# Optimization experiments

Hardware: AMD Instinct MI355X
Metric: run time of the kernel (lower is better)

The kernel has to match this reference:

```python
import jax, jax.numpy as jnp
import numpy as np

N = 50000      # nodes
E = 800000     # edges
IN_DIM = 16
D = 128        # latent_dim == d_model == num_heads*d_head
H = 8
DH = 16
DFF = 512
L = 3          # n_layers
CLAMP = 5.0
EPS = 1e-5


def _layer_norm(x, g, b):
    mu = jnp.mean(x, axis=-1, keepdims=True)
    var = jnp.mean((x - mu) ** 2, axis=-1, keepdims=True)
    return (x - mu) * jax.lax.rsqrt(var + EPS) * g + b


def setup_inputs() -> dict:
    key = jax.random.key(0)
    ks = jax.random.split(key, 16)
    def w(k, shape, fan_in):
        return jax.random.normal(k, shape, dtype=jnp.float32) * (1.0 / np.sqrt(fan_in))
    inp = {
        "nf": jax.random.normal(ks[0], (N, IN_DIM), dtype=jnp.float32),
        "src": jax.random.randint(ks[1], (E,), 0, N, dtype=jnp.int32),
        "dst": jax.random.randint(ks[2], (E,), 0, N, dtype=jnp.int32),
        "enc_W": w(ks[3], (D, IN_DIM), IN_DIM),
        "enc_b": jnp.zeros((D,), jnp.float32),
        "Wq": w(ks[4], (L, H * DH, D), D),
        "Wk": w(ks[5], (L, H * DH, D), D),
        "Wv": w(ks[6], (L, H * DH, D), D),
        "Wo": w(ks[7], (L, D, H * DH), H * DH),
        "ln1_g": jnp.ones((L, D), jnp.float32),
        "ln1_b": jnp.zeros((L, D), jnp.float32),
        "ffn_W1": w(ks[8], (L, DFF, D), D),
        "ffn_b1": jnp.zeros((L, DFF), jnp.float32),
        "ffn_W2": w(ks[9], (L, D, DFF), DFF),
        "ffn_b2": jnp.zeros((L, D), jnp.float32),
        "ln2_g": jnp.ones((L, D), jnp.float32),
        "ln2_b": jnp.zeros((L, D), jnp.float32),
        "dec_W": w(ks[10], (1, D), D),
        "dec_b": jnp.zeros((1,), jnp.float32),
    }
    return inp


def reference(nf, src, dst, enc_W, enc_b, Wq, Wk, Wv, Wo, ln1_g, ln1_b,
              ffn_W1, ffn_b1, ffn_W2, ffn_b2, ln2_g, ln2_b, dec_W, dec_b):
    h = nf @ enc_W.T + enc_b                       # [N, D]
    scale = 1.0 / np.sqrt(DH)
    for l in range(L):
        q = h @ Wq[l].T                            # [N, H*DH]
        k = h @ Wk[l].T
        v = h @ Wv[l].T
        qe = q[dst].reshape(E, H, DH)              # per-edge gather (dst query)
        ke = k[src].reshape(E, H, DH)
        u = jnp.sum(qe * ke, axis=-1) * scale      # [E, H]
        u = jnp.clip(u, -CLAMP, CLAMP)
        # edge_softmax: normalize over edges sharing the same dst node
        m = jax.ops.segment_max(u, dst, num_segments=N)   # [N, H]
        e = jnp.exp(u - m[dst])
        s = jax.ops.segment_sum(e, dst, num_segments=N)   # [N, H]
        a = e / s[dst]                             # [E, H]
        av = a[..., None] * v[src].reshape(E, H, DH)      # [E, H, DH]
        sum_av = jax.ops.segment_sum(av.reshape(E, H * DH), dst, num_segments=N)
        uh = sum_av @ Wo[l].T                      # [N, D]
        h1 = _layer_norm(h + uh, ln1_g[l], ln1_b[l])
        f = jax.nn.relu(h1 @ ffn_W1[l].T + ffn_b1[l]) @ ffn_W2[l].T + ffn_b2[l]
        h = _layer_norm(h1 + f, ln2_g[l], ln2_b[l])
    pred = h @ dec_W.T + dec_b                     # [N, 1]
    # BasicReadout('mean') over the single batched graph -> [1, 1]
    return jnp.mean(pred, axis=0, keepdims=True)
```

## Files before the change

### kernel.cpp

```cpp
#include <hip/hip_runtime.h>
#include <math.h>

static constexpr int D   = 128;
static constexpr int DFF = 512;
static constexpr int LAYERS = 3;
static constexpr float CLAMP_V = 5.0f;
static constexpr float LN_EPS = 1e-5f;

typedef unsigned short u16;
typedef unsigned int   u32;
typedef short bf16x8 __attribute__((ext_vector_type(8)));
typedef float f32x4  __attribute__((ext_vector_type(4)));

__device__ inline float4 ld4(const float* p){ return *reinterpret_cast<const float4*>(p); }
__device__ inline u16 f2bf(float f){ u32 u = __float_as_uint(f); return (u16)((u + 0x7fff + ((u>>16)&1)) >> 16); }
__device__ inline float bl(u32 u){ return __uint_as_float(u << 16); }
__device__ inline float bh(u32 u){ return __uint_as_float(u & 0xffff0000u); }

__device__ inline void gload_lds16(const void* g, void* l) {
  __builtin_amdgcn_global_load_lds(
      (const __attribute__((address_space(1))) void*)g,
      (__attribute__((address_space(3))) void*)l, 16, 0, 0);
}

__global__ __launch_bounds__(256) void count_kernel(const int* __restrict__ dst,
                                                    int* __restrict__ deg, int E)
{
  int e = blockIdx.x*256 + threadIdx.x;
  if (e < E) atomicAdd(&deg[dst[e]], 1);
}

__global__ __launch_bounds__(256) void scan_bsum(const int* __restrict__ deg,
                                                 int* __restrict__ bsum, int N)
{
  const int i0 = blockIdx.x*1024 + threadIdx.x*4;
  int s = 0;
  if (i0 + 3 < N) { int4 v = *(const int4*)&deg[i0]; s = v.x+v.y+v.z+v.w; }
  else { for (int t = 0; t < 4; t++) if (i0+t < N) s += deg[i0+t]; }
  #pragma unroll
  for (int off = 1; off < 64; off <<= 1) s += __shfl_xor(s, off);
  __shared__ int ws_[4];
  if ((threadIdx.x & 63) == 0) ws_[threadIdx.x >> 6] = s;
  __syncthreads();
  if (threadIdx.x == 0) bsum[blockIdx.x] = ws_[0]+ws_[1]+ws_[2]+ws_[3];
}

__global__ __launch_bounds__(64) void scan_bbase(int* __restrict__ bsum, int NB)
{
  const int tid = threadIdx.x;
  int base = 0;
  for (int c = 0; c < NB; c += 64) {
    const int idx = c + tid;
    int v = (idx < NB) ? bsum[idx] : 0;
    const int orig = v;
    #pragma unroll
    for (int off = 1; off < 64; off <<= 1) {
      int t = __shfl_up(v, off);
      if (tid >= off) v += t;
    }
    if (idx < NB) bsum[idx] = base + v - orig;
    base += __shfl(v, 63);
  }
}

__global__ __launch_bounds__(256) void scan_write(const int* __restrict__ deg,
    const int* __restrict__ bbase, int* __restrict__ offs, int* __restrict__ cursor, int N)
{
  const int i0 = blockIdx.x*1024 + threadIdx.x*4;
  int v[4] = {0,0,0,0};
  if (i0 + 3 < N) { int4 t = *(const int4*)&deg[i0]; v[0]=t.x; v[1]=t.y; v[2]=t.z; v[3]=t.w; }
  else { for (int t = 0; t < 4; t++) if (i0+t < N) v[t] = deg[i0+t]; }
  const int s = v[0]+v[1]+v[2]+v[3];
  const int lane = threadIdx.x & 63, w = threadIdx.x >> 6;
  int inc = s;
  #pragma unroll
  for (int off = 1; off < 64; off <<= 1) {
    int t = __shfl_up(inc, off);
    if (lane >= off) inc += t;
  }
  __shared__ int wsum[4];
  if (lane == 63) wsum[w] = inc;
  __syncthreads();
  int wb = 0;
  for (int t = 0; t < 4; t++) if (t < w) wb += wsum[t];
  int run = bbase[blockIdx.x] + wb + inc - s;
  #pragma unroll
  for (int t = 0; t < 4; t++) {
    if (i0 + t < N) { offs[i0+t] = run; cursor[i0+t] = run; run += v[t]; }
  }
  if (i0 <= N-1 && N-1 < i0+4) offs[N] = run;
}

__global__ __launch_bounds__(256) void fill_kernel(const int* __restrict__ dst,
    const int* __restrict__ src, int* __restrict__ cursor, int* __restrict__ csr_src, int E)
{
  int e = blockIdx.x*256 + threadIdx.x;
  if (e < E) {
    int p = atomicAdd(&cursor[dst[e]], 1);
    csr_src[p] = src[e];
  }
}

__global__ __launch_bounds__(256) void convert_weights(
    const float* __restrict__ Wq, const float* __restrict__ Wk, const float* __restrict__ Wv,
    const float* __restrict__ Wo, const float* __restrict__ W1, const float* __restrict__ W2,
    u16* __restrict__ out)
{
  const int SQKV = 3*384*128;
  const int SWO  = 3*128*128;
  const int SW1  = 3*512*128;
  const int SW2  = 3*128*512;
  int i = blockIdx.x*256 + threadIdx.x;
  if (i >= SQKV+SWO+SW1+SW2) return;
  float v;
  if (i < SQKV) {
    int l = i / (384*128), rem = i % (384*128);
    int row = rem / 128, col = rem % 128;
    const float* W = (row < 128) ? Wq : ((row < 256) ? Wk : Wv);
    v = W[(size_t)l*128*128 + (size_t)(row & 127)*128 + col];
  } else if (i < SQKV+SWO) {
    v = Wo[i - SQKV];
  } else if (i < SQKV+SWO+SW1) {
    v = W1[i - SQKV - SWO];
  } else {
    v = W2[i - SQKV - SWO - SW1];
  }
  out[i] = f2bf(v);
}

__global__ __launch_bounds__(256) void encoder_kernel(
    const float* __restrict__ nf, const float* __restrict__ W,
    const float* __restrict__ b, float* __restrict__ h, u16* __restrict__ hb, int N)
{
  int n = blockIdx.x*2 + (threadIdx.x >> 7);
  int d = threadIdx.x & 127;
  if (n >= N) return;
  const float* nr = nf + (size_t)n*16;
  const float* wr = W  + (size_t)d*16;
  float s = b[d];
  #pragma unroll
  for (int kk = 0; kk < 16; kk++) s = fmaf(nr[kk], wr[kk], s);
  h[(size_t)n*D + d]  = s;
  hb[(size_t)n*D + d] = f2bf(s);
}

__device__ inline void mfma_step128(const u16* __restrict__ la, const u16* __restrict__ lb,
                                    int lane, int wr, int wc, f32x4 (&acc)[4][4])
{
  #pragma unroll
  for (int k2 = 0; k2 < 2; k2++) {
    bf16x8 af[4], bfr[4];
    const int kq = k2*4 + (lane >> 4);
    #pragma unroll
    for (int mi = 0; mi < 4; mi++) {
      const int r = wr*64 + mi*16 + (lane & 15);
      af[mi] = *(const bf16x8*)&la[r*64 + ((kq ^ (r & 7)) << 3)];
    }
    #pragma unroll
    for (int ni = 0; ni < 4; ni++) {
      const int r = wc*64 + ni*16 + (lane & 15);
      bfr[ni] = *(const bf16x8*)&lb[r*64 + ((kq ^ (r & 7)) << 3)];
    }
    #pragma unroll
    for (int mi = 0; mi < 4; mi++)
      #pragma unroll
      for (int ni = 0; ni < 4; ni++)
        acc[mi][ni] = __builtin_amdgcn_mfma_f32_16x16x32_bf16(af[mi], bfr[ni], acc[mi][ni], 0, 0, 0);
  }
}

__device__ inline void mfma_stage64(const u16* __restrict__ Atile, const u16* __restrict__ Btile,
                                    int lane, int wr, int wc, int kabase, f32x4 (&acc)[2][4])
{
  #pragma unroll
  for (int k2 = 0; k2 < 2; k2++) {
    const int kql = k2*4 + (lane >> 4);
    const int kqa = kabase + kql;
    bf16x8 af[2], bfr[4];
    #pragma unroll
    for (int mi = 0; mi < 2; mi++) {
      const int r = wr*32 + mi*16 + (lane & 15);
      const int slot = ((kqa & 7) ^ (r & 7)) | (kqa & 8);
      af[mi] = *(const bf16x8*)&Atile[r*128 + slot*8];
    }
    #pragma unroll
    for (int ni = 0; ni < 4; ni++) {
      const int r = wc*64 + ni*16 + (lane & 15);
      bfr[ni] = *(const bf16x8*)&Btile[r*64 + ((kql ^ (r & 7)) << 3)];
    }
    #pragma unroll
    for (int mi = 0; mi < 2; mi++)
      #pragma unroll
      for (int ni = 0; ni < 4; ni++)
        acc[mi][ni] = __builtin_amdgcn_mfma_f32_16x16x32_bf16(af[mi], bfr[ni], acc[mi][ni], 0, 0, 0);
  }
}

__global__ __launch_bounds__(256) void gemm_qkv(
    const u16* __restrict__ A, const u16* __restrict__ B,
    float* __restrict__ qf, u16* __restrict__ kvb, int M)
{
  __shared__ u16 lA[2][128*64];
  __shared__ u16 lW[128*64];
  const int m0 = blockIdx.x * 128;
  const int tid = threadIdx.x, lane = tid & 63, wid = tid >> 6;
  const int wr = wid >> 1, wc = wid & 1;
  const int ldrow = lane >> 3;
  const int gran  = (lane & 7) ^ ldrow;

  auto issueA = [&](int ks) {
    const int k0 = ks*64 + gran*8;
    #pragma unroll
    for (int is = 0; is < 4; is++) {
      const int r = wid*32 + is*8;
      int gm = m0 + r + ldrow; if (gm >= M) gm = M - 1;
      gload_lds16(A + (size_t)gm*128 + k0, &lA[ks][r*64]);
    }
  };
  auto issueW = [&](int s) {
    const u16* Bm = B + (size_t)(s >> 1)*128*128;
    const int k0 = (s & 1)*64 + gran*8;
    #pragma unroll
    for (int is = 0; is < 4; is++) {
      const int r = wid*32 + is*8;
      gload_lds16(Bm + (size_t)(r + ldrow)*128 + k0, &lW[r*64]);
    }
  };

  issueA(0); issueA(1);

  f32x4 acc[4][4];
  const int rbase = m0 + wr*64 + ((lane >> 4) << 2);
  const int cbase = wc*64 + (lane & 15);

  #pragma unroll
  for (int s = 0; s < 6; s++) {
    issueW(s);
    asm volatile("s_waitcnt vmcnt(0)" ::: "memory");
    __syncthreads();
    if ((s & 1) == 0) {
      #pragma unroll
      for (int i = 0; i < 4; i++)
        #pragma unroll
        for (int j = 0; j < 4; j++) { acc[i][j][0]=0.f; acc[i][j][1]=0.f; acc[i][j][2]=0.f; acc[i][j][3]=0.f; }
    }
    mfma_step128(lA[s & 1], lW, lane, wr, wc, acc);
    if (s & 1) {
      const int mat = s >> 1;
      #pragma unroll
      for (int ni = 0; ni < 4; ni++) {
        const int col = cbase + ni*16;
        #pragma unroll
        for (int mi = 0; mi < 4; mi++) {
          #pragma unroll
          for (int r = 0; r < 4; r++) {
            const int gm = rbase + mi*16 + r;
            if (gm < M) {
              if (mat == 0) qf[(size_t)gm*128 + col] = acc[mi][ni][r];
              else          kvb[(size_t)gm*256 + (mat-1)*128 + col] = f2bf(acc[mi][ni][r]);
            }
          }
        }
      }
    }
    if (s < 5) __syncthreads();
  }
}

__global__ __launch_bounds__(256) void ffn_fused(
    const u16* __restrict__ savb, const u16* __restrict__ Wo,
    const u16* __restrict__ W1,   const u16* __restrict__ W2,
    const float* __restrict__ ln1g, const float* __restrict__ ln1b,
    const float* __restrict__ b1,   const float* __restrict__ b2,
    const float* __restrict__ ln2g, const float* __restrict__ ln2b,
    float* __restrict__ hf, u16* __restrict__ hb, int M)
{
  __shared__ u16 lB[128*64];
  __shared__ u16 h1s[64*128];
  __shared__ u16 fs[64*128];
  __shared__ float lsum[64][2];
  __shared__ float lsq[64][2];

  const int tid  = threadIdx.x;
  const int lane = tid & 63;
  const int wid  = tid >> 6;
  const int wr   = wid >> 1, wc = wid & 1;
  const int m0   = blockIdx.x * 64;

  const int ldrow = lane >> 3;
  const int gran  = (lane & 7) ^ ldrow;

  const int rbase_l = wr*32 + ((lane >> 4) << 2);
  const int cbase   = wc*64 + (lane & 15);

  auto stage_issue = [&](int s) {
    #pragma unroll
    for (int is = 0; is < 4; is++) {
      const int r = wid*32 + is*8;
      const u16* gp;
      if (s < 2) gp = Wo + (size_t)(r + ldrow)*128 + s*64;
      else {
        const int t = s - 2, c = t >> 2, k = t & 3;
        gp = (k < 2) ? (W1 + (size_t)(c*128 + r + ldrow)*128 + k*64)
                     : (W2 + (size_t)(r + ldrow)*512 + c*128 + (k-2)*64);
      }
      gload_lds16(gp + gran*8, &lB[r*64]);
    }
  };

  #pragma unroll
  for (int is = 0; is < 4; is++) {
    const int r0 = wid*16 + is*4;
    const int rr = r0 + (lane >> 4);
    int gm = m0 + rr; if (gm >= M) gm = M - 1;
    const int gsrc = ((lane & 7) ^ (rr & 7)) | (lane & 8);
    gload_lds16(savb + (size_t)gm*128 + gsrc*8, &fs[r0*128]);
  }

  f32x4 acc1[2][4], acc2[2][4], acc3[2][4];
  #pragma unroll
  for (int i = 0; i < 2; i++)
    #pragma unroll
    for (int j = 0; j < 4; j++) {
      acc1[i][j][0]=0.f; acc1[i][j][1]=0.f; acc1[i][j][2]=0.f; acc1[i][j][3]=0.f;
      acc3[i][j][0]=0.f; acc3[i][j][1]=0.f; acc3[i][j][2]=0.f; acc3[i][j][3]=0.f;
    }

  #pragma unroll
  for (int s = 0; s < 18; s++) {
    stage_issue(s);
    asm volatile("s_waitcnt vmcnt(0)" ::: "memory");
    __syncthreads();

    if (s >= 2 && ((s - 2) & 3) == 0) {
      #pragma unroll
      for (int i = 0; i < 2; i++)
        #pragma unroll
        for (int j = 0; j < 4; j++) { acc2[i][j][0]=0.f; acc2[i][j][1]=0.f; acc2[i][j][2]=0.f; acc2[i][j][3]=0.f; }
    }

    if (s < 2)
      mfma_stage64(fs,  lB, lane, wr, wc, (s & 1)*8, acc1);
    else if (((s - 2) & 3) < 2)
      mfma_stage64(h1s, lB, lane, wr, wc, (s & 1)*8, acc2);
    else
      mfma_stage64(fs,  lB, lane, wr, wc, (s & 1)*8, acc3);

    if (s == 1) {
      #pragma unroll
      for (int mi = 0; mi < 2; mi++) {
        #pragma unroll
        for (int r = 0; r < 4; r++) {
          const int lrow = rbase_l + mi*16 + r;
          int gr = m0 + lrow; if (gr >= M) gr = M - 1;
          float ps = 0.f, pq = 0.f;
          #pragma unroll
          for (int ni = 0; ni < 4; ni++) {
            const int col = cbase + ni*16;
            float x = acc1[mi][ni][r] + hf[(size_t)gr*128 + col];
            acc1[mi][ni][r] = x;
            ps += x; pq += x*x;
          }
          #pragma unroll
          for (int off = 1; off < 16; off <<= 1) { ps += __shfl_xor(ps, off); pq += __shfl_xor(pq, off); }
          if ((lane & 15) == 0) { lsum[lrow][wc] = ps; lsq[lrow][wc] = pq; }
        }
      }
      __syncthreads();
      #pragma unroll
      for (int mi = 0; mi < 2; mi++) {
        #pragma unroll
        for (int r = 0; r < 4; r++) {
          const int lrow = rbase_l + mi*16 + r;
          const float mean = (lsum[lrow][0] + lsum[lrow][1]) * (1.0f/128.0f);
          float var = (lsq[lrow][0] + lsq[lrow][1]) * (1.0f/128.0f) - mean*mean;
          const float rstd = rsqrtf(fmaxf(var, 0.f) + LN_EPS);
          #pragma unroll
          for (int ni = 0; ni < 4; ni++) {
            const int col = cbase + ni*16;
            float o = (acc1[mi][ni][r] - mean) * rstd * ln1g[col] + ln1b[col];
            acc1[mi][ni][r] = o;
            const int g16 = col >> 3;
            const int slot = ((g16 & 7) ^ (lrow & 7)) | (g16 & 8);
            h1s[lrow*128 + slot*8 + (col & 7)] = f2bf(o);
          }
        }
      }
    } else if (s >= 2 && ((s - 2) & 3) == 1) {
      const int c = (s - 2) >> 2;
      #pragma unroll
      for (int mi = 0; mi < 2; mi++) {
        #pragma unroll
        for (int r = 0; r < 4; r++) {
          const int lrow = rbase_l + mi*16 + r;
          #pragma unroll
          for (int ni = 0; ni < 4; ni++) {
            const int col = cbase + ni*16;
            float v = fmaxf(acc2[mi][ni][r] + b1[c*128 + col], 0.f);
            const int g16 = col >> 3;
            const int slot = ((g16 & 7) ^ (lrow & 7)) | (g16 & 8);
            fs[lrow*128 + slot*8 + (col & 7)] = f2bf(v);
          }
        }
      }
    }

    if (s < 17) __syncthreads();
  }

  #pragma unroll
  for (int mi = 0; mi < 2; mi++) {
    #pragma unroll
    for (int r = 0; r < 4; r++) {
      const int lrow = rbase_l + mi*16 + r;
      float ps = 0.f, pq = 0.f;
      #pragma unroll
      for (int ni = 0; ni < 4; ni++) {
        const int col = cbase + ni*16;
        float x = acc3[mi][ni][r] + b2[col] + acc1[mi][ni][r];
        acc3[mi][ni][r] = x;
        ps += x; pq += x*x;
      }
      #pragma unroll
      for (int off = 1; off < 16; off <<= 1) { ps += __shfl_xor(ps, off); pq += __shfl_xor(pq, off); }
      if ((lane & 15) == 0) { lsum[lrow][wc] = ps; lsq[lrow][wc] = pq; }
    }
  }
  __syncthreads();
  #pragma unroll
  for (int mi = 0; mi < 2; mi++) {
    #pragma unroll
    for (int r = 0; r < 4; r++) {
      const int lrow = rbase_l + mi*16 + r;
      const int grow = m0 + lrow;
      if (grow >= M) continue;
      const float mean = (lsum[lrow][0] + lsum[lrow][1]) * (1.0f/128.0f);
      float var = (lsq[lrow][0] + lsq[lrow][1]) * (1.0f/128.0f) - mean*mean;
      const float rstd = rsqrtf(fmaxf(var, 0.f) + LN_EPS);
      #pragma unroll
      for (int ni = 0; ni < 4; ni++) {
        const int col = cbase + ni*16;
        float o = (acc3[mi][ni][r] - mean) * rstd * ln2g[col] + ln2b[col];
        hf[(size_t)grow*128 + col] = o;
        hb[(size_t)grow*128 + col] = f2bf(o);
      }
    }
  }
}

__global__ __launch_bounds__(256) void attn_kernel(
    const float* __restrict__ q, const u16* __restrict__ kv,
    const int* __restrict__ offs, const int* __restrict__ csr_src,
    u16* __restrict__ outb, int N)
{
  const int tid = threadIdx.x;
  const int j   = tid & 15;
  const int n   = blockIdx.x*16 + (tid >> 4);
  if (n >= N) return;

  float qreg[8];
  *(float4*)&qreg[0] = ld4(&q[(size_t)n*128 + j*8]);
  *(float4*)&qreg[4] = ld4(&q[(size_t)n*128 + j*8 + 4]);

  const int start = offs[n];
  const int deg   = offs[n+1] - start;

  float s = 0.f;
  float acc[8] = {0,0,0,0,0,0,0,0};
  const int gb = tid & 48;

  for (int base = 0; base < deg; base += 16) {
    const int myidx = base + j;
    const int sn_mine = (myidx < deg) ? csr_src[start + myidx] : 0;
    const int cnt = (deg - base < 16) ? (deg - base) : 16;

    for (int b2 = 0; b2 < cnt; b2 += 8) {
      const int m8 = cnt - b2;
      uint4 K4[8], V4[8];
      #pragma unroll
      for (int u = 0; u < 8; u++) {
        const int sel = b2 + ((u < m8) ? u : 0);
        const int sn = __shfl(sn_mine, gb + sel);
        const u16* row = kv + (size_t)sn*256 + j*8;
        K4[u] = *(const uint4*)row;
        V4[u] = *(const uint4*)(row + 128);
      }
      #pragma unroll
      for (int u = 0; u < 8; u++) {
        if (u < m8) {
          float d = bl(K4[u].x)*qreg[0] + bh(K4[u].x)*qreg[1]
                  + bl(K4[u].y)*qreg[2] + bh(K4[u].y)*qreg[3]
                  + bl(K4[u].z)*qreg[4] + bh(K4[u].z)*qreg[5]
                  + bl(K4[u].w)*qreg[6] + bh(K4[u].w)*qreg[7];
          d += __shfl_xor(d, 1);
          float uu = fminf(fmaxf(d * 0.25f, -CLAMP_V), CLAMP_V);
          float e = __expf(uu - CLAMP_V);
          s += e;
          acc[0] = fmaf(e, bl(V4[u].x), acc[0]);
          acc[1] = fmaf(e, bh(V4[u].x), acc[1]);
          acc[2] = fmaf(e, bl(V4[u].y), acc[2]);
          acc[3] = fmaf(e, bh(V4[u].y), acc[3]);
          acc[4] = fmaf(e, bl(V4[u].z), acc[4]);
          acc[5] = fmaf(e, bh(V4[u].z), acc[5]);
          acc[6] = fmaf(e, bl(V4[u].w), acc[6]);
          acc[7] = fmaf(e, bh(V4[u].w), acc[7]);
        }
      }
    }
  }

  const float rs = (deg > 0) ? (1.0f / s) : 0.f;
  u16 o[8];
  #pragma unroll
  for (int t = 0; t < 8; t++) o[t] = f2bf(acc[t] * rs);
  *(uint4*)&outb[(size_t)n*128 + j*8] = *(const uint4*)o;
}

__global__ __launch_bounds__(256) void dec_partial(const float* __restrict__ h,
    const float* __restrict__ W, float* __restrict__ partials, int N)
{
  float acc = 0.f;
  for (int n = blockIdx.x*256 + threadIdx.x; n < N; n += 256*256) {
    const float* hr = h + (size_t)n*D;
    float s = 0.f;
    #pragma unroll
    for (int t = 0; t < 32; t++) {
      float4 hv = ld4(&hr[t*4]); float4 wv = ld4(&W[t*4]);
      s += hv.x*wv.x + hv.y*wv.y + hv.z*wv.z + hv.w*wv.w;
    }
    acc += s;
  }
  #pragma unroll
  for (int off = 1; off < 64; off <<= 1) acc += __shfl_xor(acc, off);
  __shared__ float red[4];
  int lane = threadIdx.x & 63, w = threadIdx.x >> 6;
  if (lane == 0) red[w] = acc;
  __syncthreads();
  if (threadIdx.x == 0) partials[blockIdx.x] = red[0]+red[1]+red[2]+red[3];
}

__global__ __launch_bounds__(256) void dec_final(const float* __restrict__ partials,
    const float* __restrict__ decb, float* __restrict__ out, int N)
{
  float a = partials[threadIdx.x];
  #pragma unroll
  for (int off = 1; off < 64; off <<= 1) a += __shfl_xor(a, off);
  __shared__ float red[4];
  int lane = threadIdx.x & 63, w = threadIdx.x >> 6;
  if (lane == 0) red[w] = a;
  __syncthreads();
  if (threadIdx.x == 0) out[0] = (red[0]+red[1]+red[2]+red[3]) / (float)N + decb[0];
}

extern "C" void kernel_launch(void* const* d_in, const int* in_sizes, int n_in,
                              void* d_out, int out_size, void* d_ws, size_t ws_size,
                              hipStream_t stream)
{
  const float* nf   = (const float*)d_in[0];
  const int*   src  = (const int*)  d_in[1];
  const int*   dst  = (const int*)  d_in[2];
  const float* encW = (const float*)d_in[3];
  const float* encb = (const float*)d_in[4];
  const float* Wq   = (const float*)d_in[5];
  const float* Wk   = (const float*)d_in[6];
  const float* Wv   = (const float*)d_in[7];
  const float* Wo   = (const float*)d_in[8];
  const float* ln1g = (const float*)d_in[9];
  const float* ln1b = (const float*)d_in[10];
  const float* W1   = (const float*)d_in[11];
  const float* b1   = (const float*)d_in[12];
  const float* W2   = (const float*)d_in[13];
  const float* b2   = (const float*)d_in[14];
  const float* ln2g = (const float*)d_in[15];
  const float* ln2b = (const float*)d_in[16];
  const float* decW = (const float*)d_in[17];
  const float* decb = (const float*)d_in[18];
  float* out = (float*)d_out;

  const int N = in_sizes[0] / 16;
  const int E = in_sizes[1];
  const int NB = (N + 1023) / 1024;

  float* ws   = (float*)d_ws;
  float* h    = ws;
  float* q    = h  + (size_t)N*128;
  u16*  hb    = (u16*)(q + (size_t)N*128);
  u16*  kvb   = hb  + (size_t)N*128;
  u16*  savb  = kvb + (size_t)N*256;
  int* deg    = (int*)(savb + (size_t)N*128);
  int* offs   = deg + N;
  int* cursor = offs + N + 1;
  int* csr    = cursor + N;
  int* bsum   = csr + E;
  float* partials = (float*)(bsum + ((NB + 255) & ~255));
  u16* wbuf   = (u16*)(partials + 512);
  u16* wqkv   = wbuf;
  u16* wo_b   = wbuf + 147456;
  u16* w1_b   = wbuf + 196608;
  u16* w2_b   = wbuf + 393216;

  hipMemsetAsync(deg, 0, sizeof(int)*N, stream);
  count_kernel<<<(E+255)/256, 256, 0, stream>>>(dst, deg, E);
  scan_bsum<<<NB, 256, 0, stream>>>(deg, bsum, N);
  scan_bbase<<<1, 64, 0, stream>>>(bsum, NB);
  scan_write<<<NB, 256, 0, stream>>>(deg, bsum, offs, cursor, N);
  fill_kernel<<<(E+255)/256, 256, 0, stream>>>(dst, src, cursor, csr, E);

  convert_weights<<<(589824+255)/256, 256, 0, stream>>>(Wq, Wk, Wv, Wo, W1, W2, wbuf);

  encoder_kernel<<<(N+1)/2, 256, 0, stream>>>(nf, encW, encb, h, hb, N);

  const int gmx = (N + 127)/128;
  for (int l = 0; l < LAYERS; l++) {
    const u16* wqkv_l = wqkv + (size_t)l*384*128;
    const u16* wo_l   = wo_b + (size_t)l*128*128;
    const u16* w1_l   = w1_b + (size_t)l*512*128;
    const u16* w2_l   = w2_b + (size_t)l*128*512;

    gemm_qkv<<<gmx, 256, 0, stream>>>(hb, wqkv_l, q, kvb, N);

    attn_kernel<<<(N+15)/16, 256, 0, stream>>>(q, kvb, offs, csr, savb, N);

    ffn_fused<<<(N+63)/64, 256, 0, stream>>>(
        savb, wo_l, w1_l, w2_l,
        ln1g + l*D, ln1b + l*D, b1 + l*DFF, b2 + l*D, ln2g + l*D, ln2b + l*D,
        h, hb, N);
  }

  dec_partial<<<256, 256, 0, stream>>>(h, decW, partials, N);
  dec_final<<<1, 256, 0, stream>>>(partials, decb, out, N);
}
```

Baseline: 545.4 us.

## Fuse next layer's QKV projection into FFN kernel epilogue

The FFN kernel now keeps the layer-norm output as bf16 in shared memory and immediately multiplies it by the next layer's Q/K/V weights, writing q and kv directly. The standalone QKV GEMM is launched only once, for the first layer. This removes two kernel launches and the write and re-read of the bf16 hidden state between kernels. In exchange the FFN kernel gets longer and uses more registers, and it no longer writes hb. The QKV stage uses 64-row tiles and a serialized load-wait-compute loop with no overlap between weight loads and MFMA work.

After: 652.9 us. 19.7% more time.

```diff
diff --git a/kernel.cpp b/kernel.cpp
--- a/kernel.cpp
+++ b/kernel.cpp
@@ -267,13 +267,15 @@
   }
 }
 
+template<bool QKV>
 __global__ __launch_bounds__(256) void ffn_fused(
     const u16* __restrict__ savb, const u16* __restrict__ Wo,
     const u16* __restrict__ W1,   const u16* __restrict__ W2,
+    const u16* __restrict__ Wqkv,
     const float* __restrict__ ln1g, const float* __restrict__ ln1b,
     const float* __restrict__ b1,   const float* __restrict__ b2,
     const float* __restrict__ ln2g, const float* __restrict__ ln2b,
-    float* __restrict__ hf, u16* __restrict__ hb, int M)
+    float* __restrict__ hf, float* __restrict__ qf, u16* __restrict__ kvb, int M)
 {
   __shared__ u16 lB[128*64];
   __shared__ u16 h1s[64*128];
@@ -433,7 +435,6 @@
     for (int r = 0; r < 4; r++) {
       const int lrow = rbase_l + mi*16 + r;
       const int grow = m0 + lrow;
-      if (grow >= M) continue;
       const float mean = (lsum[lrow][0] + lsum[lrow][1]) * (1.0f/128.0f);
       float var = (lsq[lrow][0] + lsq[lrow][1]) * (1.0f/128.0f) - mean*mean;
       const float rstd = rsqrtf(fmaxf(var, 0.f) + LN_EPS);
@@ -441,9 +442,57 @@
       for (int ni = 0; ni < 4; ni++) {
         const int col = cbase + ni*16;
         float o = (acc3[mi][ni][r] - mean) * rstd * ln2g[col] + ln2b[col];
-        hf[(size_t)grow*128 + col] = o;
-        hb[(size_t)grow*128 + col] = f2bf(o);
-      }
+        if (grow < M) hf[(size_t)grow*128 + col] = o;
+        if (QKV) {
+          const int g16 = col >> 3;
+          const int slot = ((g16 & 7) ^ (lrow & 7)) | (g16 & 8);
+          h1s[lrow*128 + slot*8 + (col & 7)] = f2bf(o);
+        }
+      }
+    }
+  }
+
+  if (QKV) {
+    auto issueQ = [&](int s) {
+      const u16* Bm = Wqkv + (size_t)(s >> 1)*128*128;
+      const int k0 = (s & 1)*64 + gran*8;
+      #pragma unroll
+      for (int is = 0; is < 4; is++) {
+        const int r = wid*32 + is*8;
+        gload_lds16(Bm + (size_t)(r + ldrow)*128 + k0, &lB[r*64]);
+      }
+    };
+    f32x4 qacc[2][4];
+    #pragma unroll
+    for (int s = 0; s < 6; s++) {
+      issueQ(s);
+      asm volatile("s_waitcnt vmcnt(0)" ::: "memory");
+      __syncthreads();
+      if ((s & 1) == 0) {
+        #pragma unroll
+        for (int i = 0; i < 2; i++)
+          #pragma unroll
+          for (int j = 0; j < 4; j++) { qacc[i][j][0]=0.f; qacc[i][j][1]=0.f; qacc[i][j][2]=0.f; qacc[i][j][3]=0.f; }
+      }
+      mfma_stage64(h1s, lB, lane, wr, wc, (s & 1)*8, qacc);
+      if (s & 1) {
+        const int mat = s >> 1;
+        #pragma unroll
+        for (int mi = 0; mi < 2; mi++) {
+          #pragma unroll
+          for (int r = 0; r < 4; r++) {
+            const int grow = m0 + rbase_l + mi*16 + r;
+            if (grow >= M) continue;
+            #pragma unroll
+            for (int ni = 0; ni < 4; ni++) {
+              const int col = cbase + ni*16;
+              if (mat == 0) qf[(size_t)grow*128 + col] = qacc[mi][ni][r];
+              else          kvb[(size_t)grow*256 + (mat-1)*128 + col] = f2bf(qacc[mi][ni][r]);
+            }
+          }
+        }
+      }
+      if (s < 5) __syncthreads();
     }
   }
 }
@@ -611,20 +660,28 @@
   encoder_kernel<<<(N+1)/2, 256, 0, stream>>>(nf, encW, encb, h, hb, N);
 
   const int gmx = (N + 127)/128;
+  const int g64 = (N + 63)/64;
+
+  gemm_qkv<<<gmx, 256, 0, stream>>>(hb, wqkv, q, kvb, N);
+
   for (int l = 0; l < LAYERS; l++) {
-    const u16* wqkv_l = wqkv + (size_t)l*384*128;
     const u16* wo_l   = wo_b + (size_t)l*128*128;
     const u16* w1_l   = w1_b + (size_t)l*512*128;
     const u16* w2_l   = w2_b + (size_t)l*128*512;
-
-    gemm_qkv<<<gmx, 256, 0, stream>>>(hb, wqkv_l, q, kvb, N);
+    const u16* wqkv_n = wqkv + (size_t)(l+1)*384*128;
 
     attn_kernel<<<(N+15)/16, 256, 0, stream>>>(q, kvb, offs, csr, savb, N);
 
-    ffn_fused<<<(N+63)/64, 256, 0, stream>>>(
-        savb, wo_l, w1_l, w2_l,
-        ln1g + l*D, ln1b + l*D, b1 + l*DFF, b2 + l*D, ln2g + l*D, ln2b + l*D,
-        h, hb, N);
+    if (l < LAYERS-1)
+      ffn_fused<true><<<g64, 256, 0, stream>>>(
+          savb, wo_l, w1_l, w2_l, wqkv_n,
+          ln1g + l*D, ln1b + l*D, b1 + l*DFF, b2 + l*D, ln2g + l*D, ln2b + l*D,
+          h, q, kvb, N);
+    else
+      ffn_fused<false><<<g64, 256, 0, stream>>>(
+          savb, wo_l, w1_l, w2_l, nullptr,
+          ln1g + l*D, ln1b + l*D, b1 + l*DFF, b2 + l*D, ln2g + l*D, ln2b + l*D,
+          h, nullptr, nullptr, N);
   }
 
   dec_partial<<<256, 256, 0, stream>>>(h, decW, partials, N);
```
